# Performance work log

Measured on AMD Instinct MI355X. Metric: run time of the kernel, lower is better.

Reference implementation:

```python
import jax, jax.numpy as jnp
import numpy as np
from jax import lax

N_NODES, IN_FEATS = 10000, 768
B, P, MAXLEN = 2048, 16384, 50
V, D, NF, HID = 50000, 300, 100, 64


def setup_inputs() -> dict:
    key = jax.random.key(0)
    ks = jax.random.split(key, 17)
    emb = jax.random.normal(ks[4], (V, D), jnp.float32) * 0.1
    emb = emb.at[0].set(0.0)  # padding_idx=0
    return {
        'x': jax.random.normal(ks[0], (N_NODES, IN_FEATS), jnp.float32),
        'rootindex': jax.random.randint(ks[1], (B,), 0, N_NODES),
        'hist_tokens': jax.random.randint(ks[2], (P, MAXLEN), 0, V),
        'segment_ids': jnp.sort(jax.random.randint(ks[3], (P,), 0, B)),
        'emb_table': emb,
        'conv_w3': jax.random.normal(ks[5], (NF, D, 3), jnp.float32) * 0.02,
        'conv_b3': jax.random.normal(ks[6], (NF,), jnp.float32) * 0.02,
        'conv_w4': jax.random.normal(ks[7], (NF, D, 4), jnp.float32) * 0.02,
        'conv_b4': jax.random.normal(ks[8], (NF,), jnp.float32) * 0.02,
        'conv_w5': jax.random.normal(ks[9], (NF, D, 5), jnp.float32) * 0.02,
        'conv_b5': jax.random.normal(ks[10], (NF,), jnp.float32) * 0.02,
        'hist_w': jax.random.normal(ks[11], (HID, 3 * NF), jnp.float32) * 0.05,
        'hist_b': jax.random.normal(ks[12], (HID,), jnp.float32) * 0.02,
        'fc_w1': jax.random.normal(ks[13], (2 * HID, IN_FEATS), jnp.float32) * 0.03,
        'fc_b1': jax.random.normal(ks[14], (2 * HID,), jnp.float32) * 0.02,
        'fc_w2': jax.random.normal(ks[15], (HID, 2 * HID), jnp.float32) * 0.08,
        'fc_b2': jax.random.normal(ks[16], (HID,), jnp.float32) * 0.02,
    }


def reference(x, rootindex, hist_tokens, segment_ids, emb_table,
              conv_w3, conv_b3, conv_w4, conv_b4, conv_w5, conv_b5,
              hist_w, hist_b, fc_w1, fc_b1, fc_w2, fc_b2):
    nseg = rootindex.shape[0]  # B users
    # --- hist_aggregation: ragged per-user embedding lookup + mean over posts ---
    emb = emb_table[hist_tokens]                                   # [P, L, D]
    sums = jax.ops.segment_sum(emb, segment_ids, num_segments=nseg)  # [B, L, D]
    counts = jax.ops.segment_sum(jnp.ones((segment_ids.shape[0],), emb.dtype),
                                 segment_ids, num_segments=nseg)
    hist = sums / jnp.maximum(counts, 1.0)[:, None, None]          # [B, L, D]
    # --- records_aggregation: TextCNN over [B, D, L] ---
    xr = jnp.transpose(hist, (0, 2, 1))                            # [B, D, L]
    feats = []
    for w, b in ((conv_w3, conv_b3), (conv_w4, conv_b4), (conv_w5, conv_b5)):
        c = lax.conv_general_dilated(xr, w, (1,), 'VALID',
                                     dimension_numbers=('NCH', 'OIH', 'NCH'))
        c = jax.nn.relu(c + b[None, :, None])                      # [B, NF, L-K+1]
        feats.append(jnp.max(c, axis=-1))                          # global max pool
    f = jnp.concatenate(feats, axis=1)                             # [B, 3*NF]
    rec = f @ hist_w.T + hist_b                                    # [B, 64]
    # --- fc_out on root node features (dropout = eval no-op) ---
    h = jax.nn.relu(x[rootindex] @ fc_w1.T + fc_b1)                # [B, 128]
    out_fc = h @ fc_w2.T + fc_b2                                   # [B, 64]
    return rec + out_fc
```

## Files before the change

kernel.cpp:

```cpp
#include <hip/hip_runtime.h>

#define NB    2048
#define NP    16384
#define LL    50
#define DD    300
#define DP    320
#define TP    52
#define NTOT  300
#define NPADF 320
#define INFEAT 768
#define HID2  128
#define UPB   4
#define FCM   16

typedef short v8s __attribute__((ext_vector_type(8)));
typedef float v4f __attribute__((ext_vector_type(4)));

__device__ __forceinline__ unsigned short f2bf(float f) {
    union { float f; unsigned u; } v; v.f = f;
    return (unsigned short)((v.u + 0x7FFF + ((v.u >> 16) & 1)) >> 16);
}
__device__ __forceinline__ float bf2f(unsigned short u) {
    union { unsigned u; float f; } v; v.u = ((unsigned)u) << 16; return v.f;
}
__device__ __forceinline__ int lower_bound_i(const int* __restrict__ a, int n, int v) {
    int lo = 0, hi = n;
    while (lo < hi) { int mid = (lo + hi) >> 1; if (a[mid] < v) lo = mid + 1; else hi = mid; }
    return lo;
}

__global__ void emb_cvt(const float* __restrict__ in, unsigned short* __restrict__ out, int n4) {
    int i = blockIdx.x * blockDim.x + threadIdx.x;
    if (i >= n4) return;
    float4 v = ((const float4*)in)[i];
    ushort4 o; o.x = f2bf(v.x); o.y = f2bf(v.y); o.z = f2bf(v.z); o.w = f2bf(v.w);
    ((ushort4*)out)[i] = o;
}

__global__ void prep_w(const float* __restrict__ w3, const float* __restrict__ w4,
                       const float* __restrict__ w5,
                       const float* __restrict__ b3, const float* __restrict__ b4,
                       const float* __restrict__ b5,
                       unsigned short* __restrict__ W5f, float* __restrict__ bias_all) {
    int idx = blockIdx.x * blockDim.x + threadIdx.x;
    if (idx < NPADF) {
        float bv = 0.f;
        if (idx < 100) bv = b3[idx];
        else if (idx < 200) bv = b4[idx - 100];
        else if (idx < 300) bv = b5[idx - 200];
        bias_all[idx] = bv;
    }
    if (idx >= 10 * 5 * 20 * 512) return;
    int j    = idx & 7;
    int lane = (idx >> 3) & 63;
    int rest = idx >> 9;
    int nt = rest % 20;
    int s  = (rest / 20) % 5;
    int kt = rest / 100;
    int col = lane & 15, quad = lane >> 4;
    int nf = nt * 16 + col;
    int d  = kt * 32 + quad * 8 + j;
    float v = 0.f;
    if (nf < NTOT && d < DD) {
        int cls = nf / 100, f = nf % 100, K = cls + 3;
        if (s < K) {
            const float* w = (cls == 0) ? w3 : (cls == 1) ? w4 : w5;
            v = w[(f * DD + d) * K + s];
        }
    }
    W5f[idx] = f2bf(v);
}

#define PCHUNK 32
__global__ __launch_bounds__(512, 1) void gather_kernel(
    const int* __restrict__ hist_tokens, const int* __restrict__ seg,
    const unsigned short* __restrict__ embb, unsigned short* __restrict__ histb)
{
    __shared__ int tokoff[PCHUNK * LL];
    const int b = blockIdx.x, tid = threadIdx.x;
    const int lo = lower_bound_i(seg, NP, b);
    const int hi = lower_bound_i(seg, NP, b + 1);
    const float inv = 1.0f / fmaxf((float)(hi - lo), 1.0f);

    int toff[8], doff[8];
    #pragma unroll
    for (int j = 0; j < 8; ++j) {
        int idx = tid + 512 * j;
        if (idx < 3750) { toff[j] = idx / 75; doff[j] = (idx % 75) * 4; }
        else            { toff[j] = 0;        doff[j] = 0; }
    }
    const bool has8 = (tid < 166);

    float4 acc[8];
    #pragma unroll
    for (int j = 0; j < 8; ++j) acc[j] = make_float4(0.f, 0.f, 0.f, 0.f);

    for (int p0 = lo; p0 < hi; p0 += PCHUNK) {
        const int pc = min(PCHUNK, hi - p0);
        __syncthreads();
        for (int j = tid; j < pc * LL; j += 512)
            tokoff[j] = hist_tokens[p0 * LL + j] * DD;
        __syncthreads();
        for (int pp = 0; pp < pc; ++pp) {
            const int* tr = tokoff + pp * LL;
            #pragma unroll
            for (int j = 0; j < 7; ++j) {
                const ushort4 v = *(const ushort4*)(embb + tr[toff[j]] + doff[j]);
                acc[j].x += bf2f(v.x); acc[j].y += bf2f(v.y);
                acc[j].z += bf2f(v.z); acc[j].w += bf2f(v.w);
            }
            if (has8) {
                const ushort4 v = *(const ushort4*)(embb + tr[toff[7]] + doff[7]);
                acc[7].x += bf2f(v.x); acc[7].y += bf2f(v.y);
                acc[7].z += bf2f(v.z); acc[7].w += bf2f(v.w);
            }
        }
    }

    unsigned short* hb = histb + (size_t)b * TP * DP;
    #pragma unroll
    for (int j = 0; j < 8; ++j) {
        if (j < 7 || has8) {
            ushort4 o;
            o.x = f2bf(acc[j].x * inv); o.y = f2bf(acc[j].y * inv);
            o.z = f2bf(acc[j].z * inv); o.w = f2bf(acc[j].w * inv);
            *(ushort4*)(hb + toff[j] * DP + doff[j]) = o;
        }
    }
    for (int i = tid; i < 640 + 1000; i += 512) {
        int t, d;
        if (i < 640) { t = 50 + i / 320; d = i % 320; }
        else         { int j = i - 640; t = j / 20; d = 300 + j % 20; }
        hb[t * DP + d] = 0;
    }
}

__global__ __launch_bounds__(512, 1) void conv_kernel(
    const unsigned short* __restrict__ histb, const unsigned short* __restrict__ W5f,
    const float* __restrict__ bias_all,
    const float* __restrict__ hist_w, const float* __restrict__ hist_b,
    float* __restrict__ out)
{
    __shared__ __align__(16) unsigned short sA[2][UPB * 52 * 40];
    __shared__ __align__(16) unsigned short sB[2][20 * 512];
    __shared__ __align__(16) float fpool[UPB * NPADF];

    const int b = blockIdx.x, tid = threadIdx.x;
    const int wave = tid >> 6, lane = tid & 63;
    const int col = lane & 15, quad = lane >> 4;
    const int u = wave >> 1, h = wave & 1;

    const unsigned short* hbase = histb + (size_t)(b * UPB) * TP * DP;

    const int c0 = tid, c1 = tid + 512;
    const int a0_uu = c0 / 208, a0_r = c0 % 208;
    const int a0_row = a0_r >> 2, a0_ch = a0_r & 3;
    const int a1_uu = c1 / 208, a1_r = c1 % 208;
    const int a1_row = a1_r >> 2, a1_ch = a1_r & 3;
    const bool hasA1 = (c1 < 832);
    const bool hasB2 = (tid < 256);

    v4f acc[3][10];
    #pragma unroll
    for (int m = 0; m < 3; ++m)
        #pragma unroll
        for (int n = 0; n < 10; ++n)
            acc[m][n] = (v4f){0.f, 0.f, 0.f, 0.f};

    {
        v8s a0 = *(const v8s*)(hbase + (size_t)a0_uu * TP * DP + a0_row * DP + a0_ch * 8);
        v8s a1v;
        if (hasA1) a1v = *(const v8s*)(hbase + (size_t)a1_uu * TP * DP + a1_row * DP + a1_ch * 8);
        v8s t0 = *(const v8s*)(W5f + (size_t)tid * 8);
        v8s t1 = *(const v8s*)(W5f + (size_t)(tid + 512) * 8);
        v8s t2;
        if (hasB2) t2 = *(const v8s*)(W5f + (size_t)(tid + 1024) * 8);
        *(v8s*)(sA[0] + (a0_uu * 52 + a0_row) * 40 + a0_ch * 8) = a0;
        if (hasA1) *(v8s*)(sA[0] + (a1_uu * 52 + a1_row) * 40 + a1_ch * 8) = a1v;
        *(v8s*)(sB[0] + tid * 8) = t0;
        *(v8s*)(sB[0] + (tid + 512) * 8) = t1;
        if (hasB2) *(v8s*)(sB[0] + (tid + 1024) * 8) = t2;
    }

    const int bread_off = (h * 10) * 512 + lane * 8;

    for (int kt = 0; kt < 10; ++kt) {
        const unsigned short* Abuf = sA[kt & 1];
        for (int s = 0; s < 5; ++s) {
            const int step = kt * 5 + s;
            __syncthreads();

            v8s t0, t1, t2;
            const bool haveB = (step < 49);
            if (haveB) {
                const unsigned short* gb = W5f + (size_t)(step + 1) * 10240;
                t0 = *(const v8s*)(gb + tid * 8);
                t1 = *(const v8s*)(gb + (tid + 512) * 8);
                if (hasB2) t2 = *(const v8s*)(gb + (tid + 1024) * 8);
            }
            v8s a0v, a1v;
            const bool haveA = (s == 4) && (kt < 9);
            if (haveA) {
                const int ko = (kt + 1) * 32;
                a0v = *(const v8s*)(hbase + (size_t)a0_uu * TP * DP + a0_row * DP + ko + a0_ch * 8);
                if (hasA1)
                    a1v = *(const v8s*)(hbase + (size_t)a1_uu * TP * DP + a1_row * DP + ko + a1_ch * 8);
            }

            const unsigned short* Bbuf = sB[step & 1];
            v8s a[3];
            #pragma unroll
            for (int m = 0; m < 3; ++m)
                a[m] = *(const v8s*)(Abuf + (u * 52 + m * 16 + col + s) * 40 + quad * 8);
            v8s bf[10];
            #pragma unroll
            for (int n = 0; n < 10; ++n)
                bf[n] = *(const v8s*)(Bbuf + bread_off + n * 512);
            #pragma unroll
            for (int n = 0; n < 10; ++n)
                #pragma unroll
                for (int m = 0; m < 3; ++m)
                    acc[m][n] = __builtin_amdgcn_mfma_f32_16x16x32_bf16(a[m], bf[n], acc[m][n], 0, 0, 0);

            if (haveB) {
                unsigned short* db = sB[(step + 1) & 1];
                *(v8s*)(db + tid * 8) = t0;
                *(v8s*)(db + (tid + 512) * 8) = t1;
                if (hasB2) *(v8s*)(db + (tid + 1024) * 8) = t2;
            }
            if (haveA) {
                unsigned short* da = sA[(kt + 1) & 1];
                *(v8s*)(da + (a0_uu * 52 + a0_row) * 40 + a0_ch * 8) = a0v;
                if (hasA1) *(v8s*)(da + (a1_uu * 52 + a1_row) * 40 + a1_ch * 8) = a1v;
            }
        }
    }

    __syncthreads();
    #pragma unroll
    for (int n = 0; n < 10; ++n) {
        const int nf = (h * 10 + n) * 16 + col;
        const int Tout = 48 - nf / 100;
        float mx = -1e30f;
        #pragma unroll
        for (int m = 0; m < 3; ++m)
            #pragma unroll
            for (int r = 0; r < 4; ++r) {
                int t = m * 16 + quad * 4 + r;
                if (t < Tout) mx = fmaxf(mx, acc[m][n][r]);
            }
        mx = fmaxf(mx, __shfl_xor(mx, 16, 64));
        mx = fmaxf(mx, __shfl_xor(mx, 32, 64));
        if (quad == 0 && nf < NTOT)
            fpool[u * NPADF + nf] = fmaxf(0.f, mx + bias_all[nf]);
    }
    __syncthreads();

    if (tid < UPB * 64) {
        const int uu = tid >> 6, o = tid & 63;
        const float4* fw = (const float4*)(hist_w + o * NTOT);
        const float4* fp = (const float4*)(fpool + uu * NPADF);
        float s = 0.f;
        #pragma unroll
        for (int q = 0; q < NTOT / 4; ++q) {
            float4 aa = fp[q], ww = fw[q];
            s += aa.x * ww.x + aa.y * ww.y + aa.z * ww.z + aa.w * ww.w;
        }
        out[(b * UPB + uu) * 64 + o] = s + hist_b[o];
    }
}

__global__ __launch_bounds__(256, 1) void fc_mfma(
    const float* __restrict__ x, const int* __restrict__ rootindex,
    const unsigned short* __restrict__ w1b, const float* __restrict__ b1,
    const float* __restrict__ w2, const float* __restrict__ b2,
    float* __restrict__ out)
{
    __shared__ __align__(16) unsigned short sA[FCM * 72];
    __shared__ __align__(16) float hl[FCM * 132];
    __shared__ __align__(16) float w2l[64 * 129];
    __shared__ int roots[FCM];

    const int b = blockIdx.x, tid = threadIdx.x;
    if (tid < FCM) roots[tid] = rootindex[b * FCM + tid];
    for (int i = tid; i < 64 * HID2; i += 256)
        w2l[(i >> 7) * 129 + (i & 127)] = w2[i];
    __syncthreads();

    const int wave = tid >> 6, lane = tid & 63;
    const int col = lane & 15, quad = lane >> 4;

    v4f acc[2];
    acc[0] = (v4f){0.f, 0.f, 0.f, 0.f};
    acc[1] = (v4f){0.f, 0.f, 0.f, 0.f};

    const int r_st = tid >> 4, q_st = tid & 15;

    for (int kt = 0; kt < 12; ++kt) {
        __syncthreads();
        float4 v = *(const float4*)(x + (size_t)roots[r_st] * INFEAT + kt * 64 + q_st * 4);
        ushort4 o; o.x = f2bf(v.x); o.y = f2bf(v.y); o.z = f2bf(v.z); o.w = f2bf(v.w);
        *(ushort4*)(sA + r_st * 72 + q_st * 4) = o;
        __syncthreads();
        #pragma unroll
        for (int kc = 0; kc < 2; ++kc) {
            const v8s a = *(const v8s*)(sA + col * 72 + kc * 32 + quad * 8);
            #pragma unroll
            for (int n = 0; n < 2; ++n) {
                const int nf = (wave * 2 + n) * 16 + col;
                const v8s bfr = *(const v8s*)(w1b + (size_t)nf * INFEAT + kt * 64 + kc * 32 + quad * 8);
                acc[n] = __builtin_amdgcn_mfma_f32_16x16x32_bf16(a, bfr, acc[n], 0, 0, 0);
            }
        }
    }

    #pragma unroll
    for (int nt = 0; nt < 2; ++nt) {
        const int n = (wave * 2 + nt) * 16 + col;
        const float bv = b1[n];
        #pragma unroll
        for (int r = 0; r < 4; ++r)
            hl[(quad * 4 + r) * 132 + n] = fmaxf(acc[nt][r] + bv, 0.f);
    }
    __syncthreads();

    {
        const int o = tid & 63, ug = tid >> 6;
        const float b2v = b2[o];
        const float* wrow = w2l + o * 129;
        #pragma unroll
        for (int i = 0; i < 4; ++i) {
            const int u = ug * 4 + i;
            const float* hrow = hl + u * 132;
            float s = 0.f;
            #pragma unroll 16
            for (int k = 0; k < HID2; ++k) s += hrow[k] * wrow[k];
            out[(b * FCM + u) * 64 + o] += s + b2v;
        }
    }
}

extern "C" void kernel_launch(void* const* d_in, const int* in_sizes, int n_in,
                              void* d_out, int out_size, void* d_ws, size_t ws_size,
                              hipStream_t stream) {
    const float* x        = (const float*)d_in[0];
    const int*   rootidx  = (const int*)d_in[1];
    const int*   hist_tok = (const int*)d_in[2];
    const int*   seg      = (const int*)d_in[3];
    const float* emb      = (const float*)d_in[4];
    const float* w3       = (const float*)d_in[5];
    const float* cb3      = (const float*)d_in[6];
    const float* w4       = (const float*)d_in[7];
    const float* cb4      = (const float*)d_in[8];
    const float* w5       = (const float*)d_in[9];
    const float* cb5      = (const float*)d_in[10];
    const float* hist_w   = (const float*)d_in[11];
    const float* hist_b   = (const float*)d_in[12];
    const float* fw1      = (const float*)d_in[13];
    const float* fb1      = (const float*)d_in[14];
    const float* fw2      = (const float*)d_in[15];
    const float* fb2      = (const float*)d_in[16];
    float* out = (float*)d_out;

    char* ws = (char*)d_ws;
    unsigned short* emb_bf  = (unsigned short*)(ws);
    unsigned short* hist_bf = (unsigned short*)(ws + 30000000);
    unsigned short* W5f     = (unsigned short*)(ws + 98157440);
    float*          bias_all= (float*)(ws + 99181440);
    unsigned short* w1b     = (unsigned short*)(ws + 99182720);

    emb_cvt<<<(50000 * DD / 4 + 255) / 256, 256, 0, stream>>>(emb, emb_bf, 50000 * DD / 4);
    emb_cvt<<<(HID2 * INFEAT / 4 + 255) / 256, 256, 0, stream>>>(fw1, w1b, HID2 * INFEAT / 4);
    prep_w<<<(10 * 5 * 20 * 512 + 255) / 256, 256, 0, stream>>>(w3, w4, w5, cb3, cb4, cb5, W5f, bias_all);
    gather_kernel<<<NB, 512, 0, stream>>>(hist_tok, seg, emb_bf, hist_bf);
    conv_kernel<<<NB / UPB, 512, 0, stream>>>(hist_bf, W5f, bias_all, hist_w, hist_b, out);
    fc_mfma<<<NB / FCM, 256, 0, stream>>>(x, rootidx, w1b, fb1, fw2, fb2, out);
}
```

Before: 352.4 us.

## Restructure conv kernel to 12 waves with single-buffered LDS and tap-skipping

```diff
diff --git a/kernel.cpp b/kernel.cpp
--- a/kernel.cpp
+++ b/kernel.cpp
@@ -135,124 +135,116 @@
     }
 }
 
-__global__ __launch_bounds__(512, 1) void conv_kernel(
+__global__ __launch_bounds__(768, 3) void conv_kernel(
     const unsigned short* __restrict__ histb, const unsigned short* __restrict__ W5f,
     const float* __restrict__ bias_all,
     const float* __restrict__ hist_w, const float* __restrict__ hist_b,
     float* __restrict__ out)
 {
-    __shared__ __align__(16) unsigned short sA[2][UPB * 52 * 40];
-    __shared__ __align__(16) unsigned short sB[2][20 * 512];
+    __shared__ __align__(16) unsigned short sA[UPB * 52 * 40];
+    __shared__ __align__(16) unsigned short sB[19 * 512];
     __shared__ __align__(16) float fpool[UPB * NPADF];
 
     const int b = blockIdx.x, tid = threadIdx.x;
     const int wave = tid >> 6, lane = tid & 63;
     const int col = lane & 15, quad = lane >> 4;
-    const int u = wave >> 1, h = wave & 1;
+    const int u = wave & 3, g = wave >> 2;
+    const int base = (g == 2) ? 14 : g * 7;
+    const int cnt  = (g == 2) ? 5  : 7;
 
     const unsigned short* hbase = histb + (size_t)(b * UPB) * TP * DP;
 
-    const int c0 = tid, c1 = tid + 512;
+    const int c0 = tid;
     const int a0_uu = c0 / 208, a0_r = c0 % 208;
     const int a0_row = a0_r >> 2, a0_ch = a0_r & 3;
+    const int c1 = tid + 768;
     const int a1_uu = c1 / 208, a1_r = c1 % 208;
     const int a1_row = a1_r >> 2, a1_ch = a1_r & 3;
-    const bool hasA1 = (c1 < 832);
-    const bool hasB2 = (tid < 256);
-
-    v4f acc[3][10];
+    const bool hasA1 = (tid < 64);
+
+    v4f acc[3][7];
     #pragma unroll
     for (int m = 0; m < 3; ++m)
         #pragma unroll
-        for (int n = 0; n < 10; ++n)
-            acc[m][n] = (v4f){0.f, 0.f, 0.f, 0.f};
-
-    {
-        v8s a0 = *(const v8s*)(hbase + (size_t)a0_uu * TP * DP + a0_row * DP + a0_ch * 8);
-        v8s a1v;
-        if (hasA1) a1v = *(const v8s*)(hbase + (size_t)a1_uu * TP * DP + a1_row * DP + a1_ch * 8);
-        v8s t0 = *(const v8s*)(W5f + (size_t)tid * 8);
-        v8s t1 = *(const v8s*)(W5f + (size_t)(tid + 512) * 8);
-        v8s t2;
-        if (hasB2) t2 = *(const v8s*)(W5f + (size_t)(tid + 1024) * 8);
-        *(v8s*)(sA[0] + (a0_uu * 52 + a0_row) * 40 + a0_ch * 8) = a0;
-        if (hasA1) *(v8s*)(sA[0] + (a1_uu * 52 + a1_row) * 40 + a1_ch * 8) = a1v;
-        *(v8s*)(sB[0] + tid * 8) = t0;
-        *(v8s*)(sB[0] + (tid + 512) * 8) = t1;
-        if (hasB2) *(v8s*)(sB[0] + (tid + 1024) * 8) = t2;
-    }
-
-    const int bread_off = (h * 10) * 512 + lane * 8;
+        for (int j = 0; j < 7; ++j)
+            acc[m][j] = (v4f){0.f, 0.f, 0.f, 0.f};
+
+    v8s t0 = {}, t1 = {}, a0v = {}, a1v = {};
+    a0v = *(const v8s*)(hbase + (size_t)a0_uu * TP * DP + a0_row * DP + a0_ch * 8);
+    if (hasA1)
+        a1v = *(const v8s*)(hbase + (size_t)a1_uu * TP * DP + a1_row * DP + a1_ch * 8);
+    t0 = *(const v8s*)(W5f + (size_t)tid * 8);
+    if (tid < 448) t1 = *(const v8s*)(W5f + (size_t)(tid + 768) * 8);
 
     for (int kt = 0; kt < 10; ++kt) {
-        const unsigned short* Abuf = sA[kt & 1];
+        #pragma unroll
         for (int s = 0; s < 5; ++s) {
             const int step = kt * 5 + s;
+            const int lo   = (s == 3) ? 6 : (s == 4) ? 12 : 0;
+            const int Cc   = (19 - lo) * 64;
+
             __syncthreads();
-
-            v8s t0, t1, t2;
-            const bool haveB = (step < 49);
-            if (haveB) {
-                const unsigned short* gb = W5f + (size_t)(step + 1) * 10240;
-                t0 = *(const v8s*)(gb + tid * 8);
-                t1 = *(const v8s*)(gb + (tid + 512) * 8);
-                if (hasB2) t2 = *(const v8s*)(gb + (tid + 1024) * 8);
-            }
-            v8s a0v, a1v;
-            const bool haveA = (s == 4) && (kt < 9);
-            if (haveA) {
+            if (s == 0) {
+                *(v8s*)(sA + (a0_uu * 52 + a0_row) * 40 + a0_ch * 8) = a0v;
+                if (hasA1) *(v8s*)(sA + (a1_uu * 52 + a1_row) * 40 + a1_ch * 8) = a1v;
+            }
+            {
+                unsigned short* db = sB + lo * 512;
+                if (tid < Cc)       *(v8s*)(db + tid * 8) = t0;
+                if (tid + 768 < Cc) *(v8s*)(db + (tid + 768) * 8) = t1;
+            }
+            __syncthreads();
+
+            if ((s < 4) || (kt < 9)) {
+                const int sn  = (s == 4) ? 0 : s + 1;
+                const int lon = (sn == 3) ? 6 : (sn == 4) ? 12 : 0;
+                const int Cn  = (19 - lon) * 64;
+                const unsigned short* gb = W5f + (size_t)(step + 1) * 10240 + lon * 512;
+                if (tid < Cn)       t0 = *(const v8s*)(gb + tid * 8);
+                if (tid + 768 < Cn) t1 = *(const v8s*)(gb + (tid + 768) * 8);
+            }
+            if (s == 4 && kt < 9) {
                 const int ko = (kt + 1) * 32;
                 a0v = *(const v8s*)(hbase + (size_t)a0_uu * TP * DP + a0_row * DP + ko + a0_ch * 8);
                 if (hasA1)
                     a1v = *(const v8s*)(hbase + (size_t)a1_uu * TP * DP + a1_row * DP + ko + a1_ch * 8);
             }
 
-            const unsigned short* Bbuf = sB[step & 1];
-            v8s a[3];
+            const unsigned short* Arow = sA + (u * 52 + col + s) * 40 + quad * 8;
+            const v8s am0 = *(const v8s*)(Arow);
+            const v8s am1 = *(const v8s*)(Arow + 640);
+            const v8s am2 = *(const v8s*)(Arow + 1280);
+            #pragma unroll
+            for (int j = 0; j < 7; ++j) {
+                const int t = base + j;
+                if (j < cnt && t >= lo) {
+                    const v8s bf = *(const v8s*)(sB + t * 512 + lane * 8);
+                    acc[0][j] = __builtin_amdgcn_mfma_f32_16x16x32_bf16(am0, bf, acc[0][j], 0, 0, 0);
+                    acc[1][j] = __builtin_amdgcn_mfma_f32_16x16x32_bf16(am1, bf, acc[1][j], 0, 0, 0);
+                    acc[2][j] = __builtin_amdgcn_mfma_f32_16x16x32_bf16(am2, bf, acc[2][j], 0, 0, 0);
+                }
+            }
+        }
+    }
+
+    #pragma unroll
+    for (int j = 0; j < 7; ++j) {
+        if (j < cnt) {
+            const int nf = (base + j) * 16 + col;
+            const int Tout = 48 - nf / 100;
+            float mx = -1e30f;
             #pragma unroll
             for (int m = 0; m < 3; ++m)
-                a[m] = *(const v8s*)(Abuf + (u * 52 + m * 16 + col + s) * 40 + quad * 8);
-            v8s bf[10];
-            #pragma unroll
-            for (int n = 0; n < 10; ++n)
-                bf[n] = *(const v8s*)(Bbuf + bread_off + n * 512);
-            #pragma unroll
-            for (int n = 0; n < 10; ++n)
                 #pragma unroll
-                for (int m = 0; m < 3; ++m)
-                    acc[m][n] = __builtin_amdgcn_mfma_f32_16x16x32_bf16(a[m], bf[n], acc[m][n], 0, 0, 0);
-
-            if (haveB) {
-                unsigned short* db = sB[(step + 1) & 1];
-                *(v8s*)(db + tid * 8) = t0;
-                *(v8s*)(db + (tid + 512) * 8) = t1;
-                if (hasB2) *(v8s*)(db + (tid + 1024) * 8) = t2;
-            }
-            if (haveA) {
-                unsigned short* da = sA[(kt + 1) & 1];
-                *(v8s*)(da + (a0_uu * 52 + a0_row) * 40 + a0_ch * 8) = a0v;
-                if (hasA1) *(v8s*)(da + (a1_uu * 52 + a1_row) * 40 + a1_ch * 8) = a1v;
-            }
-        }
-    }
-
-    __syncthreads();
-    #pragma unroll
-    for (int n = 0; n < 10; ++n) {
-        const int nf = (h * 10 + n) * 16 + col;
-        const int Tout = 48 - nf / 100;
-        float mx = -1e30f;
-        #pragma unroll
-        for (int m = 0; m < 3; ++m)
-            #pragma unroll
-            for (int r = 0; r < 4; ++r) {
-                int t = m * 16 + quad * 4 + r;
-                if (t < Tout) mx = fmaxf(mx, acc[m][n][r]);
-            }
-        mx = fmaxf(mx, __shfl_xor(mx, 16, 64));
-        mx = fmaxf(mx, __shfl_xor(mx, 32, 64));
-        if (quad == 0 && nf < NTOT)
-            fpool[u * NPADF + nf] = fmaxf(0.f, mx + bias_all[nf]);
+                for (int r = 0; r < 4; ++r) {
+                    const int t = m * 16 + quad * 4 + r;
+                    if (t < Tout) mx = fmaxf(mx, acc[m][j][r]);
+                }
+            mx = fmaxf(mx, __shfl_xor(mx, 16, 64));
+            mx = fmaxf(mx, __shfl_xor(mx, 32, 64));
+            if (quad == 0 && nf < NTOT)
+                fpool[u * NPADF + nf] = fmaxf(0.f, mx + bias_all[nf]);
+        }
     }
     __syncthreads();
 
@@ -260,13 +252,13 @@
         const int uu = tid >> 6, o = tid & 63;
         const float4* fw = (const float4*)(hist_w + o * NTOT);
         const float4* fp = (const float4*)(fpool + uu * NPADF);
-        float s = 0.f;
+        float sum = 0.f;
         #pragma unroll
         for (int q = 0; q < NTOT / 4; ++q) {
             float4 aa = fp[q], ww = fw[q];
-            s += aa.x * ww.x + aa.y * ww.y + aa.z * ww.z + aa.w * ww.w;
-        }
-        out[(b * UPB + uu) * 64 + o] = s + hist_b[o];
+            sum += aa.x * ww.x + aa.y * ww.y + aa.z * ww.z + aa.w * ww.w;
+        }
+        out[(b * UPB + uu) * 64 + o] = sum + hist_b[o];
     }
 }
 
@@ -373,6 +365,6 @@
     emb_cvt<<<(HID2 * INFEAT / 4 + 255) / 256, 256, 0, stream>>>(fw1, w1b, HID2 * INFEAT / 4);
     prep_w<<<(10 * 5 * 20 * 512 + 255) / 256, 256, 0, stream>>>(w3, w4, w5, cb3, cb4, cb5, W5f, bias_all);
     gather_kernel<<<NB, 512, 0, stream>>>(hist_tok, seg, emb_bf, hist_bf);
-    conv_kernel<<<NB / UPB, 512, 0, stream>>>(hist_bf, W5f, bias_all, hist_w, hist_b, out);
+    conv_kernel<<<NB / UPB, 768, 0, stream>>>(hist_bf, W5f, bias_all, hist_w, hist_b, out);
     fc_mfma<<<NB / FCM, 256, 0, stream>>>(x, rootidx, w1b, fb1, fw2, fb2, out);
 }
```

New measurement: 350.4 us. No clear change (-0.5%).
